# Kernel optimization log

Hardware: AMD Instinct MI355X
Metric: run time of the kernel (lower is better)

The kernel has to match this reference:

```python
import jax, jax.numpy as jnp
import numpy as np

B, L, D = 2, 2048, 1024
H = 16
DH = D // H
FACTOR = 0.6
U = max(1, min(L, int(FACTOR * L)))  # 1228 selected queries


def setup_inputs() -> dict:
    key = jax.random.key(0)
    ks = jax.random.split(key, 9)
    s = 0.02
    return {
        "x": jax.random.normal(ks[0], (B, L, D), dtype=jnp.float32),
        "Wq": jax.random.normal(ks[1], (D, D), dtype=jnp.float32) * s,
        "bq": jnp.zeros((D,), dtype=jnp.float32),
        "Wk": jax.random.normal(ks[2], (D, D), dtype=jnp.float32) * s,
        "bk": jnp.zeros((D,), dtype=jnp.float32),
        "Wv": jax.random.normal(ks[3], (D, D), dtype=jnp.float32) * s,
        "bv": jnp.zeros((D,), dtype=jnp.float32),
        "Wo": jax.random.normal(ks[4], (D, D), dtype=jnp.float32) * s,
        "bo": jnp.zeros((D,), dtype=jnp.float32),
    }


def _split_heads(x):
    b, l, d = x.shape
    return x.reshape(b, l, H, DH).transpose(0, 2, 1, 3)  # [b,h,l,dh]


def reference(x, Wq, bq, Wk, bk, Wv, bv, Wo, bo):
    b, l, _ = x.shape
    scale = 1.0 / jnp.sqrt(jnp.asarray(DH, dtype=x.dtype))

    q = _split_heads(x @ Wq + bq)  # [b,h,l,dh]
    k = _split_heads(x @ Wk + bk)
    v = _split_heads(x @ Wv + bv)

    # full scores for sparsity heuristic
    scores = jnp.einsum("bhqd,bhkd->bhqk", q, k) * scale  # [b,h,l,l]
    sparsity = scores.max(axis=-1) - scores.mean(axis=-1)  # [b,h,l]

    _, top_idx = jax.lax.top_k(sparsity, U)  # [b,h,U]

    # gather selected queries, attend only on those rows
    q_sel = jnp.take_along_axis(q, top_idx[..., None], axis=2)  # [b,h,U,dh]
    scores_sel = jnp.einsum("bhud,bhkd->bhuk", q_sel, k) * scale  # [b,h,U,l]
    attn = jax.nn.softmax(scores_sel, axis=-1)
    out_sel = jnp.einsum("bhuk,bhkd->bhud", attn, v)  # [b,h,U,dh]

    # scatter back into zero-initialized output
    bi = jnp.arange(b)[:, None, None]
    hi = jnp.arange(H)[None, :, None]
    out = jnp.zeros_like(q).at[bi, hi, top_idx].set(out_sel)  # [b,h,l,dh]

    out = out.transpose(0, 2, 1, 3).reshape(b, l, D)
    return out @ Wo + bo
```

## Files before the change

kernel.cpp:

```cpp
#include <hip/hip_runtime.h>
#include <math.h>
#include <stdint.h>

#define Bn 2
#define Ln 2048
#define Dn 1024
#define Hn 16
#define DHn 64
#define Un 1228
#define BHn (Bn*Hn)
#define SCALE 0.125f
#define SXf 16.0f
#define SWf 256.0f
#define SQf 16.0f
#define SVf 16.0f
#define SPf 16.0f
#define ESC_PROJ (1.0f / 4096.0f)
#define ESC_OUT  (1.0f / 65536.0f)
#define PSC (SCALE / 256.0f)

typedef _Float16 f16;
typedef __attribute__((ext_vector_type(8))) _Float16 f16x8;
typedef __attribute__((ext_vector_type(4))) float f32x4;
struct h4s { f16 x, y, z, w; };

__device__ __forceinline__ void splitf16(float f, f16& hi, f16& lo) {
  hi = (f16)f;
  lo = (f16)(f - (float)hi);
}

__device__ __forceinline__ void gl_lds16(const void* g, void* l) {
  __builtin_amdgcn_global_load_lds(
      (const __attribute__((address_space(1))) void*)g,
      (__attribute__((address_space(3))) void*)l, 16, 0, 0);
}

#define MFMA(a, b, c) __builtin_amdgcn_mfma_f32_16x16x32_f16((a), (b), (c), 0, 0, 0)

__global__ __launch_bounds__(256) void split_kernel(
    const float* __restrict__ in, f16* __restrict__ oh, f16* __restrict__ ol, int n4) {
  int i = blockIdx.x * 256 + threadIdx.x;
  if (i >= n4) return;
  float4 v = ((const float4*)in)[i];
  h4s h, l;
  splitf16(v.x * SXf, h.x, l.x); splitf16(v.y * SXf, h.y, l.y);
  splitf16(v.z * SXf, h.z, l.z); splitf16(v.w * SXf, h.w, l.w);
  ((h4s*)oh)[i] = h; ((h4s*)ol)[i] = l;
}

__global__ __launch_bounds__(256) void tsplit_w4(
    const float* __restrict__ W0, const float* __restrict__ W1,
    const float* __restrict__ W2, const float* __restrict__ W3,
    f16* __restrict__ oh, f16* __restrict__ ol) {
  __shared__ float ts[64][65];
  const int t = threadIdx.x;
  const int r0 = blockIdx.x * 64, c0 = blockIdx.y * 64;
  const int z = blockIdx.z;
  const float* in = (z == 0) ? W0 : (z == 1) ? W1 : (z == 2) ? W2 : W3;
#pragma unroll
  for (int c = 0; c < 4; ++c) {
    int f = (c * 256 + t) * 4; int row = f >> 6, col = f & 63;
    float4 v = *(const float4*)&in[(size_t)(r0 + row) * Dn + c0 + col];
    ts[row][col] = v.x; ts[row][col + 1] = v.y; ts[row][col + 2] = v.z; ts[row][col + 3] = v.w;
  }
  __syncthreads();
#pragma unroll
  for (int c = 0; c < 4; ++c) {
    int f = (c * 256 + t) * 4; int crow = f >> 6, rcol = f & 63;
    h4s h, l;
    splitf16(ts[rcol + 0][crow] * SWf, h.x, l.x);
    splitf16(ts[rcol + 1][crow] * SWf, h.y, l.y);
    splitf16(ts[rcol + 2][crow] * SWf, h.z, l.z);
    splitf16(ts[rcol + 3][crow] * SWf, h.w, l.w);
    size_t o = (size_t)(z * 1024 + c0 + crow) * Dn + r0 + rcol;
    *(h4s*)&oh[o] = h; *(h4s*)&ol[o] = l;
  }
}

__global__ void gemm_qkv(
    const f16* __restrict__ Ah, const f16* __restrict__ Al,
    const f16* __restrict__ Bth, const f16* __restrict__ Btl,
    const float* __restrict__ bq, const float* __restrict__ bk, const float* __restrict__ bv,
    float* __restrict__ Qf, f16* __restrict__ Qbh, f16* __restrict__ Qbl,
    float* __restrict__ Kf, f16* __restrict__ Kbh, f16* __restrict__ Kbl,
    f16* __restrict__ Vh16, int K) {
  __shared__ f16 sAh[128 * 32], sAl[128 * 32], sBh[128 * 32], sBl[128 * 32];
  const int t = threadIdx.x;
  const int w = t >> 6, lane = t & 63, lm = lane & 15, q = lane >> 4;
  const int wr = w >> 1, wc = w & 1;
  const int n0 = blockIdx.x * 128, m0 = blockIdx.y * 128;
  f32x4 acc[4][4] = {};
  for (int k0 = 0; k0 < K; k0 += 32) {
    const f16* s0 = Ah + (size_t)m0 * K + k0;
    const f16* s1 = Al + (size_t)m0 * K + k0;
    const f16* s2 = Bth + (size_t)n0 * K + k0;
    const f16* s3 = Btl + (size_t)n0 * K + k0;
#pragma unroll
    for (int c = 0; c < 2; ++c) {
      int f = (c * 256 + t) * 8; int row = f >> 5, col = f & 31;
      size_t go = (size_t)row * K + col;
      gl_lds16(s0 + go, &sAh[f]);
      gl_lds16(s1 + go, &sAl[f]);
      gl_lds16(s2 + go, &sBh[f]);
      gl_lds16(s3 + go, &sBl[f]);
    }
    __syncthreads();
    f16x8 a_h[4], a_l[4], b_h[4], b_l[4];
#pragma unroll
    for (int mi = 0; mi < 4; ++mi) {
      int r = (wr * 64 + mi * 16 + lm) * 32 + q * 8;
      a_h[mi] = *(const f16x8*)&sAh[r];
      a_l[mi] = *(const f16x8*)&sAl[r];
    }
#pragma unroll
    for (int ni = 0; ni < 4; ++ni) {
      int r = (wc * 64 + ni * 16 + lm) * 32 + q * 8;
      b_h[ni] = *(const f16x8*)&sBh[r];
      b_l[ni] = *(const f16x8*)&sBl[r];
    }
#pragma unroll
    for (int mi = 0; mi < 4; ++mi)
#pragma unroll
      for (int ni = 0; ni < 4; ++ni) {
        acc[mi][ni] = MFMA(a_h[mi], b_h[ni], acc[mi][ni]);
        acc[mi][ni] = MFMA(a_h[mi], b_l[ni], acc[mi][ni]);
        acc[mi][ni] = MFMA(a_l[mi], b_h[ni], acc[mi][ni]);
      }
    __syncthreads();
  }
#pragma unroll
  for (int mi = 0; mi < 4; ++mi)
#pragma unroll
    for (int ni = 0; ni < 4; ++ni) {
      int nglob = n0 + wc * 64 + ni * 16;
      int seg = nglob >> 10;
      int c = (nglob & 1023) + lm;
      const float* bp = (seg == 0) ? bq : (seg == 1) ? bk : bv;
      float bvv = bp[c];
#pragma unroll
      for (int r = 0; r < 4; ++r) {
        int grow = m0 + wr * 64 + mi * 16 + q * 4 + r;
        float v = acc[mi][ni][r] * ESC_PROJ + bvv;
        size_t o = (size_t)grow * 1024 + c;
        if (seg == 0) {
          Qf[o] = v;
          f16 hh, ll; splitf16(v * SQf, hh, ll); Qbh[o] = hh; Qbl[o] = ll;
        } else if (seg == 1) {
          Kf[o] = v;
          f16 hh, ll; splitf16(v * SQf, hh, ll); Kbh[o] = hh; Kbl[o] = ll;
        } else {
          Vh16[o] = (f16)(v * SVf);
        }
      }
    }
}

__global__ __launch_bounds__(256) void tsplit_v(
    const f16* __restrict__ Vh16, f16* __restrict__ out) {
  __shared__ f16 ts[64][72];
  const int t = threadIdx.x;
  const int l0 = blockIdx.x * 64;
  const int bh = blockIdx.y, b = bh >> 4, h = bh & 15;
#pragma unroll
  for (int c = 0; c < 2; ++c) {
    int e = c * 256 + t; int row = e >> 3, cg = e & 7;
    *(uint4*)&ts[row][cg * 8] =
        *(const uint4*)&Vh16[((size_t)b * Ln + l0 + row) * Dn + h * DHn + cg * 8];
  }
  __syncthreads();
#pragma unroll
  for (int c = 0; c < 2; ++c) {
    int e = c * 256 + t; int drow = e >> 3, lg = e & 7;
    f16 tmp[8];
#pragma unroll
    for (int j = 0; j < 8; ++j) tmp[j] = ts[lg * 8 + j][drow];
    *(uint4*)&out[((size_t)bh * DHn + drow) * Ln + l0 + lg * 8] = *(uint4*)tmp;
  }
}

__global__ __launch_bounds__(256, 4) void gemm_a1(
    const f16* __restrict__ A,
    const f16* __restrict__ Bth, const f16* __restrict__ Btl,
    const float* __restrict__ bias, float escale,
    float* __restrict__ Cf, int M, int N, int K) {
  __shared__ f16 sA[128 * 32], sBh[64 * 32], sBl[64 * 32];
  const int t = threadIdx.x;
  const int w = t >> 6, lane = t & 63, lm = lane & 15, q = lane >> 4;
  const int wr = w >> 1, wc = w & 1;
  const int n0 = blockIdx.x * 64, m0 = blockIdx.y * 128;
  f32x4 acc[4][2] = {};
  for (int k0 = 0; k0 < K; k0 += 32) {
    const f16* s0 = A + (size_t)m0 * K + k0;
    const f16* s2 = Bth + (size_t)n0 * K + k0;
    const f16* s3 = Btl + (size_t)n0 * K + k0;
#pragma unroll
    for (int c = 0; c < 2; ++c) {
      int f = (c * 256 + t) * 8; int row = f >> 5, col = f & 31;
      gl_lds16(s0 + (size_t)row * K + col, &sA[f]);
    }
    {
      int f = t * 8; int row = f >> 5, col = f & 31;
      gl_lds16(s2 + (size_t)row * K + col, &sBh[f]);
      gl_lds16(s3 + (size_t)row * K + col, &sBl[f]);
    }
    __syncthreads();
    f16x8 a_[4], b_h[2], b_l[2];
#pragma unroll
    for (int mi = 0; mi < 4; ++mi)
      a_[mi] = *(const f16x8*)&sA[(wr * 64 + mi * 16 + lm) * 32 + q * 8];
#pragma unroll
    for (int ni = 0; ni < 2; ++ni) {
      int r = (wc * 32 + ni * 16 + lm) * 32 + q * 8;
      b_h[ni] = *(const f16x8*)&sBh[r];
      b_l[ni] = *(const f16x8*)&sBl[r];
    }
#pragma unroll
    for (int mi = 0; mi < 4; ++mi)
#pragma unroll
      for (int ni = 0; ni < 2; ++ni) {
        acc[mi][ni] = MFMA(a_[mi], b_h[ni], acc[mi][ni]);
        acc[mi][ni] = MFMA(a_[mi], b_l[ni], acc[mi][ni]);
      }
    __syncthreads();
  }
#pragma unroll
  for (int mi = 0; mi < 4; ++mi)
#pragma unroll
    for (int ni = 0; ni < 2; ++ni) {
      int gcol = n0 + wc * 32 + ni * 16 + lm;
      float bvv = bias[gcol];
#pragma unroll
      for (int r = 0; r < 4; ++r) {
        int grow = m0 + wr * 64 + mi * 16 + q * 4 + r;
        Cf[(size_t)grow * N + gcol] = acc[mi][ni][r] * escale + bvv;
      }
    }
}

__global__ __launch_bounds__(256) void ksum_part(
    const f16* __restrict__ Kh, const f16* __restrict__ Kl, float* __restrict__ ksum) {
  __shared__ float red[4][64];
  const int t = threadIdx.x, d = t & 63, seg = t >> 6;
  const int bx = blockIdx.x, bh = blockIdx.y, b = bh >> 4, h = bh & 15;
  float s = 0.f;
  const int lbase = bx * 256 + seg * 64;
  for (int r = 0; r < 64; ++r) {
    size_t o = ((size_t)b * Ln + lbase + r) * Dn + h * DHn + d;
    s += (float)Kh[o] + (float)Kl[o];
  }
  red[seg][d] = s;
  __syncthreads();
  if (t < 64) atomicAdd(&ksum[bh * DHn + t], red[0][t] + red[1][t] + red[2][t] + red[3][t]);
}

__global__ __launch_bounds__(256, 2) void attn_stats_mfma(
    const f16* __restrict__ Qh, const f16* __restrict__ Ql,
    const f16* __restrict__ Kh, const f16* __restrict__ Kl,
    const float* __restrict__ ksum,
    float* __restrict__ row_max, float* __restrict__ spars) {
  __shared__ f16 sQh[128 * 64], sQl[128 * 64], sKh[128 * 64], sKl[128 * 64];
  __shared__ float redm[128][5];
  const int t = threadIdx.x;
  const int w = t >> 6, lane = t & 63, lm = lane & 15, q = lane >> 4;
  const int bh = blockIdx.y, b = bh >> 4, h = bh & 15;
  const int q0 = blockIdx.x * 128;
  const f16* qsh = Qh + ((size_t)b * Ln + q0) * Dn + h * DHn;
  const f16* qsl = Ql + ((size_t)b * Ln + q0) * Dn + h * DHn;
#pragma unroll
  for (int c = 0; c < 4; ++c) {
    int f = (c * 256 + t) * 8; int row = f >> 6, col = f & 63;
    size_t go = (size_t)row * Dn + col;
    gl_lds16(qsh + go, &sQh[f]);
    gl_lds16(qsl + go, &sQl[f]);
  }
  __syncthreads();
  f16x8 a_h[8][2], a_l[8][2];
#pragma unroll
  for (int mi = 0; mi < 8; ++mi)
#pragma unroll
    for (int ks = 0; ks < 2; ++ks) {
      int r = (mi * 16 + lm) * 64 + ks * 32 + q * 8;
      a_h[mi][ks] = *(const f16x8*)&sQh[r];
      a_l[mi][ks] = *(const f16x8*)&sQl[r];
    }
  float rmax[8][4];
#pragma unroll
  for (int mi = 0; mi < 8; ++mi)
#pragma unroll
    for (int r = 0; r < 4; ++r) rmax[mi][r] = -1e30f;

  for (int kt = 0; kt < Ln / 128; ++kt) {
    __syncthreads();
    const f16* ksh = Kh + ((size_t)b * Ln + kt * 128) * Dn + h * DHn;
    const f16* ksl = Kl + ((size_t)b * Ln + kt * 128) * Dn + h * DHn;
#pragma unroll
    for (int c = 0; c < 4; ++c) {
      int f = (c * 256 + t) * 8; int row = f >> 6, col = f & 63;
      size_t go = (size_t)row * Dn + col;
      gl_lds16(ksh + go, &sKh[f]);
      gl_lds16(ksl + go, &sKl[f]);
    }
    __syncthreads();
#pragma unroll
    for (int ni = 0; ni < 2; ++ni) {
      int bcol = (w * 2 + ni) * 16;
      f16x8 b_h[2], b_l[2];
#pragma unroll
      for (int ks = 0; ks < 2; ++ks) {
        int r = (bcol + lm) * 64 + ks * 32 + q * 8;
        b_h[ks] = *(const f16x8*)&sKh[r];
        b_l[ks] = *(const f16x8*)&sKl[r];
      }
#pragma unroll
      for (int mi = 0; mi < 8; ++mi) {
        f32x4 acc = {0.f, 0.f, 0.f, 0.f};
#pragma unroll
        for (int ks = 0; ks < 2; ++ks) {
          acc = MFMA(a_h[mi][ks], b_h[ks], acc);
          acc = MFMA(a_h[mi][ks], b_l[ks], acc);
          acc = MFMA(a_l[mi][ks], b_h[ks], acc);
        }
#pragma unroll
        for (int r = 0; r < 4; ++r) rmax[mi][r] = fmaxf(rmax[mi][r], acc[r]);
      }
    }
  }
#pragma unroll
  for (int mi = 0; mi < 8; ++mi)
#pragma unroll
    for (int r = 0; r < 4; ++r) {
      float v = rmax[mi][r];
      v = fmaxf(v, __shfl_xor(v, 1)); v = fmaxf(v, __shfl_xor(v, 2));
      v = fmaxf(v, __shfl_xor(v, 4)); v = fmaxf(v, __shfl_xor(v, 8));
      if (lm == 0) redm[mi * 16 + q * 4 + r][w] = v;
    }
  __syncthreads();
  if (t < 128) {
    float m = fmaxf(fmaxf(redm[t][0], redm[t][1]), fmaxf(redm[t][2], redm[t][3]));
    float dot = 0.f;
    const float* kp = ksum + bh * DHn;
#pragma unroll
    for (int d = 0; d < 64; ++d)
      dot += ((float)sQh[t * 64 + d] + (float)sQl[t * 64 + d]) * kp[d];
    row_max[(size_t)bh * Ln + q0 + t] = m * PSC;
    spars[(size_t)bh * Ln + q0 + t] = m * PSC - dot * (PSC / (float)Ln);
  }
}

__global__ __launch_bounds__(1024) void topk_sort(
    const float* __restrict__ spars, int* __restrict__ top_idx, int* __restrict__ wrow) {
  __shared__ unsigned long long keys[Ln];
  const int t = threadIdx.x;
  const int bh = blockIdx.x;
  for (int i = t; i < Ln; i += 1024) {
    unsigned u = __float_as_uint(spars[(size_t)bh * Ln + i]);
    u = (u & 0x80000000u) ? ~u : (u | 0x80000000u);
    u = ~u;
    keys[i] = ((unsigned long long)u << 32) | (unsigned)i;
  }
  __syncthreads();
  for (int k = 2; k <= Ln; k <<= 1) {
    for (int j = k >> 1; j > 0; j >>= 1) {
      int i = ((t & ~(j - 1)) << 1) | (t & (j - 1));
      int ixj = i | j;
      unsigned long long a = keys[i], bb = keys[ixj];
      bool up = ((i & k) == 0);
      if ((a > bb) == up) { keys[i] = bb; keys[ixj] = a; }
      __syncthreads();
    }
  }
  for (int u = t; u < Un - 8; u += 1024)
    top_idx[(size_t)bh * Un + u] = (int)(keys[u] & 0xFFFFFFFFu);
  if (t < 16) wrow[bh * 16 + t] = (int)(keys[Un - 8 + t] & 0xFFFFFFFFu);
}

__global__ __launch_bounds__(256) void refine_rows(
    const float* __restrict__ Qf, const float* __restrict__ Kf,
    const int* __restrict__ wrow, float* __restrict__ spx) {
  __shared__ float qs[64];
  __shared__ float redm[4], reds[4];
  const int t = threadIdx.x;
  const int j = blockIdx.x, bh = blockIdx.y, b = bh >> 4, h = bh & 15;
  const int qi = wrow[bh * 16 + j];
  if (t < 64) qs[t] = Qf[((size_t)b * Ln + qi) * Dn + h * DHn + t];
  __syncthreads();
  float mx = -1e30f, sm = 0.f;
  for (int ki = t; ki < Ln; ki += 256) {
    const float* kp = &Kf[((size_t)b * Ln + ki) * Dn + h * DHn];
    float s = 0.f;
#pragma unroll
    for (int d0 = 0; d0 < 64; d0 += 4) {
      float4 k4 = *(const float4*)&kp[d0];
      s = fmaf(k4.x, qs[d0], s);
      s = fmaf(k4.y, qs[d0 + 1], s);
      s = fmaf(k4.z, qs[d0 + 2], s);
      s = fmaf(k4.w, qs[d0 + 3], s);
    }
    mx = fmaxf(mx, s); sm += s;
  }
  const int w = t >> 6, lane = t & 63;
#pragma unroll
  for (int off = 1; off < 64; off <<= 1) {
    mx = fmaxf(mx, __shfl_xor(mx, off));
    sm += __shfl_xor(sm, off);
  }
  if (lane == 0) { redm[w] = mx; reds[w] = sm; }
  __syncthreads();
  if (t == 0) {
    float m = fmaxf(fmaxf(redm[0], redm[1]), fmaxf(redm[2], redm[3]));
    float s = reds[0] + reds[1] + reds[2] + reds[3];
    spx[bh * 16 + j] = SCALE * (m - s * (1.0f / (float)Ln));
  }
}

__global__ __launch_bounds__(64) void topk_final(
    const float* __restrict__ spx, const int* __restrict__ wrow,
    int* __restrict__ top_idx) {
  const int bh = blockIdx.x;
  if (threadIdx.x != 0) return;
  float v[16]; int r[16];
#pragma unroll
  for (int j = 0; j < 16; ++j) { v[j] = spx[bh * 16 + j]; r[j] = wrow[bh * 16 + j]; }
  unsigned taken = 0;
  for (int s = 0; s < 8; ++s) {
    int best = -1;
    for (int j = 0; j < 16; ++j) {
      if (taken & (1u << j)) continue;
      if (best < 0 || v[j] > v[best] || (v[j] == v[best] && r[j] < r[best])) best = j;
    }
    taken |= 1u << best;
    top_idx[(size_t)bh * Un + (Un - 8) + s] = r[best];
  }
}

__global__ __launch_bounds__(256, 4) void attn_sel_part(
    const f16* __restrict__ Qh, const f16* __restrict__ Kh,
    const f16* __restrict__ Vth,
    const int* __restrict__ topi, const float* __restrict__ row_max,
    float* __restrict__ pO, float* __restrict__ pD) {
  __shared__ f16 sK[64 * 64], sV[64 * 64];
  __shared__ f16 sQP[64 * 80];
  __shared__ float rmL[64];
  __shared__ int qxL[64];
  __shared__ float dred[64][5];
  const int t = threadIdx.x;
  const int w = t >> 6, lane = t & 63, lm = lane & 15, q = lane >> 4;
  const int half = blockIdx.y & 1, bh = blockIdx.y >> 1, b = bh >> 4, h = bh & 15;
  const int u0 = blockIdx.x * 64;
  const int nrows = (Un - u0 < 64) ? (Un - u0) : 64;
  if (t < 64) {
    int qi = topi[(size_t)bh * Un + ((t < nrows) ? (u0 + t) : 0)];
    qxL[t] = qi;
    rmL[t] = row_max[(size_t)bh * Ln + qi];
  }
  __syncthreads();
#pragma unroll
  for (int c = 0; c < 2; ++c) {
    int f = (c * 256 + t) * 8; int row = f >> 6, col = f & 63;
    size_t go = ((size_t)b * Ln + qxL[row]) * Dn + h * DHn + col;
    *(uint4*)&sQP[row * 80 + col] = *(const uint4*)&Qh[go];
  }
  __syncthreads();
  f16x8 aq[4][2];
#pragma unroll
  for (int mi = 0; mi < 4; ++mi)
#pragma unroll
    for (int ks = 0; ks < 2; ++ks)
      aq[mi][ks] = *(const f16x8*)&sQP[(mi * 16 + lm) * 80 + ks * 32 + q * 8];
  f32x4 oacc[4] = {};
  float dacc[4][4] = {};

  const f16* kbase = Kh + (size_t)b * Ln * Dn + h * DHn;
  const f16* vbase = Vth + (size_t)bh * DHn * Ln;
  for (int kt = 0; kt < 16; ++kt) {
    const int l0 = half * 1024 + kt * 64;
    __syncthreads();
#pragma unroll
    for (int c = 0; c < 2; ++c) {
      int f = (c * 256 + t) * 8; int row = f >> 6, col = f & 63;
      gl_lds16(kbase + (size_t)(l0 + row) * Dn + col, &sK[f]);
      gl_lds16(vbase + (size_t)row * Ln + l0 + col, &sV[f]);
    }
    __syncthreads();
    f16x8 kb[2];
#pragma unroll
    for (int ks = 0; ks < 2; ++ks)
      kb[ks] = *(const f16x8*)&sK[(w * 16 + lm) * 64 + ks * 32 + q * 8];
#pragma unroll
    for (int mi = 0; mi < 4; ++mi) {
      f32x4 acc = {0.f, 0.f, 0.f, 0.f};
      acc = MFMA(aq[mi][0], kb[0], acc);
      acc = MFMA(aq[mi][1], kb[1], acc);
#pragma unroll
      for (int r = 0; r < 4; ++r) {
        int row = mi * 16 + q * 4 + r;
        float p = __expf(acc[r] * PSC - rmL[row]);
        dacc[mi][r] += p;
        sQP[row * 80 + w * 16 + lm] = (f16)(p * SPf);
      }
    }
    __syncthreads();
    f16x8 vb[2];
#pragma unroll
    for (int ks = 0; ks < 2; ++ks)
      vb[ks] = *(const f16x8*)&sV[(w * 16 + lm) * 64 + ks * 32 + q * 8];
#pragma unroll
    for (int mi = 0; mi < 4; ++mi) {
#pragma unroll
      for (int ks = 0; ks < 2; ++ks) {
        f16x8 pf = *(const f16x8*)&sQP[(mi * 16 + lm) * 80 + ks * 32 + q * 8];
        oacc[mi] = MFMA(pf, vb[ks], oacc[mi]);
      }
    }
  }
#pragma unroll
  for (int mi = 0; mi < 4; ++mi)
#pragma unroll
    for (int r = 0; r < 4; ++r) {
      float v = dacc[mi][r];
      v += __shfl_xor(v, 1); v += __shfl_xor(v, 2);
      v += __shfl_xor(v, 4); v += __shfl_xor(v, 8);
      if (lm == 0) dred[mi * 16 + q * 4 + r][w] = v;
    }
  __syncthreads();
  const size_t pbase = ((size_t)half * BHn + bh) * 1280 + u0;
  if (t < 64)
    pD[pbase + t] = dred[t][0] + dred[t][1] + dred[t][2] + dred[t][3];
#pragma unroll
  for (int mi = 0; mi < 4; ++mi)
#pragma unroll
    for (int r = 0; r < 4; ++r) {
      int row = mi * 16 + q * 4 + r;
      pO[(pbase + row) * 64 + w * 16 + lm] = oacc[mi][r];
    }
}

__global__ __launch_bounds__(256) void attn_combine(
    const float* __restrict__ pO, const float* __restrict__ pD,
    const int* __restrict__ topi, f16* __restrict__ AOh) {
  const int t = threadIdx.x;
  const int u0 = blockIdx.x * 64, bh = blockIdx.y, b = bh >> 4, h = bh & 15;
  const int nrows = (Un - u0 < 64) ? (Un - u0) : 64;
  const int row = t >> 2, pg = t & 3;
  if (row >= nrows) return;
  int qi = topi[(size_t)bh * Un + u0 + row];
  size_t i0 = (size_t)bh * 1280 + u0 + row;
  size_t i1 = (size_t)BHn * 1280 + i0;
  float dinv = 1.0f / (pD[i0] + pD[i1]);
  const float* p0 = &pO[i0 * 64 + pg * 16];
  const float* p1 = &pO[i1 * 64 + pg * 16];
  f16 buf[16];
#pragma unroll
  for (int c = 0; c < 4; ++c) {
    float4 a = *(const float4*)&p0[c * 4];
    float4 bb = *(const float4*)&p1[c * 4];
    buf[c * 4 + 0] = (f16)((a.x + bb.x) * dinv);
    buf[c * 4 + 1] = (f16)((a.y + bb.y) * dinv);
    buf[c * 4 + 2] = (f16)((a.z + bb.z) * dinv);
    buf[c * 4 + 3] = (f16)((a.w + bb.w) * dinv);
  }
  f16* dst = &AOh[((size_t)b * Ln + qi) * Dn + h * DHn + pg * 16];
  *(uint4*)&dst[0] = *(uint4*)&buf[0];
  *(uint4*)&dst[8] = *(uint4*)&buf[8];
}

extern "C" void kernel_launch(void* const* d_in, const int* in_sizes, int n_in,
                              void* d_out, int out_size, void* d_ws, size_t ws_size,
                              hipStream_t stream) {
  (void)in_sizes; (void)n_in; (void)out_size; (void)ws_size;
  const float* x  = (const float*)d_in[0];
  const float* Wq = (const float*)d_in[1];
  const float* bq = (const float*)d_in[2];
  const float* Wk = (const float*)d_in[3];
  const float* bk = (const float*)d_in[4];
  const float* Wv = (const float*)d_in[5];
  const float* bv = (const float*)d_in[6];
  const float* Wo = (const float*)d_in[7];
  const float* bo = (const float*)d_in[8];
  float* out = (float*)d_out;

  uint8_t* p = (uint8_t*)d_ws;
  const size_t NE = (size_t)Bn * Ln * Dn;
  f16* xh = (f16*)p;  p += NE * 2;
  f16* xl = (f16*)p;  p += NE * 2;
  f16* Wt_h = (f16*)p; p += (size_t)4096 * Dn * 2;
  f16* Wt_l = (f16*)p; p += (size_t)4096 * Dn * 2;
  f16* Qbh = (f16*)p; p += NE * 2;
  f16* Qbl = (f16*)p; p += NE * 2;
  f16* Kbh = (f16*)p; p += NE * 2;
  f16* Kbl = (f16*)p; p += NE * 2;
  float* Qf = (float*)p;  p += NE * 4;
  float* Kf = (float*)p;  p += NE * 4;
  f16* Vh16 = (f16*)p; p += NE * 2;
  f16* Vth  = (f16*)p; p += NE * 2;
  float* rowmax = (float*)p; p += (size_t)BHn * Ln * 4;
  float* spars  = (float*)p; p += (size_t)BHn * Ln * 4;
  float* ksum   = (float*)p; p += (size_t)BHn * DHn * 4;
  int* topi     = (int*)p;   p += (size_t)BHn * Un * 4;
  int* wrow     = (int*)p;   p += (size_t)BHn * 16 * 4;
  float* spx    = (float*)p; p += (size_t)BHn * 16 * 4;
  float* pD     = (float*)p; p += (size_t)2 * BHn * 1280 * 4;
  float* pO = Qf;
  f16* AOh = xh;

  dim3 blk(256);
  hipLaunchKernelGGL(split_kernel, dim3((int)(NE / 4 / 256)), blk, 0, stream, x, xh, xl, (int)(NE / 4));
  hipLaunchKernelGGL(tsplit_w4, dim3(16, 16, 4), blk, 0, stream, Wq, Wk, Wv, Wo, Wt_h, Wt_l);
  hipLaunchKernelGGL(gemm_qkv, dim3(24, 32), blk, 0, stream, xh, xl, Wt_h, Wt_l,
                     bq, bk, bv, Qf, Qbh, Qbl, Kf, Kbh, Kbl, Vh16, Dn);
  hipLaunchKernelGGL(tsplit_v, dim3(Ln / 64, BHn), blk, 0, stream, Vh16, Vth);
  hipMemsetAsync(ksum, 0, (size_t)BHn * DHn * 4, stream);
  hipLaunchKernelGGL(ksum_part, dim3(8, BHn), blk, 0, stream, Kbh, Kbl, ksum);
  hipLaunchKernelGGL(attn_stats_mfma, dim3(Ln / 128, BHn), blk, 0, stream,
                     Qbh, Qbl, Kbh, Kbl, ksum, rowmax, spars);
  hipLaunchKernelGGL(topk_sort, dim3(BHn), dim3(1024), 0, stream, spars, topi, wrow);
  hipLaunchKernelGGL(refine_rows, dim3(16, BHn), blk, 0, stream, Qf, Kf, wrow, spx);
  hipLaunchKernelGGL(topk_final, dim3(BHn), dim3(64), 0, stream, spx, wrow, topi);
  hipMemsetAsync(AOh, 0, NE * 2, stream);
  hipLaunchKernelGGL(attn_sel_part, dim3((Un + 63) / 64, 2 * BHn), blk, 0, stream,
                     Qbh, Kbh, Vth, topi, rowmax, pO, pD);
  hipLaunchKernelGGL(attn_combine, dim3((Un + 63) / 64, BHn), blk, 0, stream,
                     pO, pD, topi, AOh);
  hipLaunchKernelGGL(gemm_a1, dim3(16, 32), blk, 0, stream, AOh,
                     Wt_h + (size_t)3072 * Dn, Wt_l + (size_t)3072 * Dn, bo,
                     ESC_OUT, out, Bn * Ln, Dn, Dn);
}
```

Measured before the change: 406.7 us.

## Drop split-fp16 low parts for Q/K scoring and widen refinement window

Sparsity scoring in attn_stats_mfma now uses plain fp16 Q and K with a single MFMA per k-step instead of three split-precision MFMAs. This removes the Qbl/Kbl buffers and their writes and halves LDS use, which allows higher occupancy (launch bounds raised to 4 blocks). ksum now reads fp32 K directly. To offset the loss of precision near the top-k boundary, the fp32 refinement window grows from 16 to 32 candidate rows. The risk is misselected queries if fp16 error exceeds what the wider window covers.

```diff
diff --git a/kernel.cpp b/kernel.cpp
--- a/kernel.cpp
+++ b/kernel.cpp
@@ -9,6 +9,7 @@
 #define DHn 64
 #define Un 1228
 #define BHn (Bn*Hn)
+#define WIN 32
 #define SCALE 0.125f
 #define SXf 16.0f
 #define SWf 256.0f
@@ -81,8 +82,8 @@
     const f16* __restrict__ Ah, const f16* __restrict__ Al,
     const f16* __restrict__ Bth, const f16* __restrict__ Btl,
     const float* __restrict__ bq, const float* __restrict__ bk, const float* __restrict__ bv,
-    float* __restrict__ Qf, f16* __restrict__ Qbh, f16* __restrict__ Qbl,
-    float* __restrict__ Kf, f16* __restrict__ Kbh, f16* __restrict__ Kbl,
+    float* __restrict__ Qf, f16* __restrict__ Qbh,
+    float* __restrict__ Kf, f16* __restrict__ Kbh,
     f16* __restrict__ Vh16, int K) {
   __shared__ f16 sAh[128 * 32], sAl[128 * 32], sBh[128 * 32], sBl[128 * 32];
   const int t = threadIdx.x;
@@ -144,10 +145,10 @@
         size_t o = (size_t)grow * 1024 + c;
         if (seg == 0) {
           Qf[o] = v;
-          f16 hh, ll; splitf16(v * SQf, hh, ll); Qbh[o] = hh; Qbl[o] = ll;
+          Qbh[o] = (f16)(v * SQf);
         } else if (seg == 1) {
           Kf[o] = v;
-          f16 hh, ll; splitf16(v * SQf, hh, ll); Kbh[o] = hh; Kbl[o] = ll;
+          Kbh[o] = (f16)(v * SQf);
         } else {
           Vh16[o] = (f16)(v * SVf);
         }
@@ -238,51 +239,42 @@
 }
 
 __global__ __launch_bounds__(256) void ksum_part(
-    const f16* __restrict__ Kh, const f16* __restrict__ Kl, float* __restrict__ ksum) {
+    const float* __restrict__ Kf, float* __restrict__ ksum) {
   __shared__ float red[4][64];
   const int t = threadIdx.x, d = t & 63, seg = t >> 6;
   const int bx = blockIdx.x, bh = blockIdx.y, b = bh >> 4, h = bh & 15;
   float s = 0.f;
   const int lbase = bx * 256 + seg * 64;
-  for (int r = 0; r < 64; ++r) {
-    size_t o = ((size_t)b * Ln + lbase + r) * Dn + h * DHn + d;
-    s += (float)Kh[o] + (float)Kl[o];
-  }
+  for (int r = 0; r < 64; ++r)
+    s += Kf[((size_t)b * Ln + lbase + r) * Dn + h * DHn + d];
   red[seg][d] = s;
   __syncthreads();
   if (t < 64) atomicAdd(&ksum[bh * DHn + t], red[0][t] + red[1][t] + red[2][t] + red[3][t]);
 }
 
-__global__ __launch_bounds__(256, 2) void attn_stats_mfma(
-    const f16* __restrict__ Qh, const f16* __restrict__ Ql,
-    const f16* __restrict__ Kh, const f16* __restrict__ Kl,
+__global__ __launch_bounds__(256, 4) void attn_stats_mfma(
+    const f16* __restrict__ Qh, const f16* __restrict__ Kh,
     const float* __restrict__ ksum,
     float* __restrict__ row_max, float* __restrict__ spars) {
-  __shared__ f16 sQh[128 * 64], sQl[128 * 64], sKh[128 * 64], sKl[128 * 64];
+  __shared__ f16 sQ[128 * 64], sK[128 * 64];
   __shared__ float redm[128][5];
   const int t = threadIdx.x;
   const int w = t >> 6, lane = t & 63, lm = lane & 15, q = lane >> 4;
   const int bh = blockIdx.y, b = bh >> 4, h = bh & 15;
   const int q0 = blockIdx.x * 128;
-  const f16* qsh = Qh + ((size_t)b * Ln + q0) * Dn + h * DHn;
-  const f16* qsl = Ql + ((size_t)b * Ln + q0) * Dn + h * DHn;
+  const f16* qs = Qh + ((size_t)b * Ln + q0) * Dn + h * DHn;
 #pragma unroll
   for (int c = 0; c < 4; ++c) {
     int f = (c * 256 + t) * 8; int row = f >> 6, col = f & 63;
-    size_t go = (size_t)row * Dn + col;
-    gl_lds16(qsh + go, &sQh[f]);
-    gl_lds16(qsl + go, &sQl[f]);
-  }
-  __syncthreads();
-  f16x8 a_h[8][2], a_l[8][2];
+    gl_lds16(qs + (size_t)row * Dn + col, &sQ[f]);
+  }
+  __syncthreads();
+  f16x8 a_[8][2];
 #pragma unroll
   for (int mi = 0; mi < 8; ++mi)
 #pragma unroll
-    for (int ks = 0; ks < 2; ++ks) {
-      int r = (mi * 16 + lm) * 64 + ks * 32 + q * 8;
-      a_h[mi][ks] = *(const f16x8*)&sQh[r];
-      a_l[mi][ks] = *(const f16x8*)&sQl[r];
-    }
+    for (int ks = 0; ks < 2; ++ks)
+      a_[mi][ks] = *(const f16x8*)&sQ[(mi * 16 + lm) * 64 + ks * 32 + q * 8];
   float rmax[8][4];
 #pragma unroll
   for (int mi = 0; mi < 8; ++mi)
@@ -291,35 +283,25 @@
 
   for (int kt = 0; kt < Ln / 128; ++kt) {
     __syncthreads();
-    const f16* ksh = Kh + ((size_t)b * Ln + kt * 128) * Dn + h * DHn;
-    const f16* ksl = Kl + ((size_t)b * Ln + kt * 128) * Dn + h * DHn;
+    const f16* ks_ = Kh + ((size_t)b * Ln + kt * 128) * Dn + h * DHn;
 #pragma unroll
     for (int c = 0; c < 4; ++c) {
       int f = (c * 256 + t) * 8; int row = f >> 6, col = f & 63;
-      size_t go = (size_t)row * Dn + col;
-      gl_lds16(ksh + go, &sKh[f]);
-      gl_lds16(ksl + go, &sKl[f]);
+      gl_lds16(ks_ + (size_t)row * Dn + col, &sK[f]);
     }
     __syncthreads();
 #pragma unroll
     for (int ni = 0; ni < 2; ++ni) {
       int bcol = (w * 2 + ni) * 16;
-      f16x8 b_h[2], b_l[2];
-#pragma unroll
-      for (int ks = 0; ks < 2; ++ks) {
-        int r = (bcol + lm) * 64 + ks * 32 + q * 8;
-        b_h[ks] = *(const f16x8*)&sKh[r];
-        b_l[ks] = *(const f16x8*)&sKl[r];
-      }
+      f16x8 b_[2];
+#pragma unroll
+      for (int ks = 0; ks < 2; ++ks)
+        b_[ks] = *(const f16x8*)&sK[(bcol + lm) * 64 + ks * 32 + q * 8];
 #pragma unroll
       for (int mi = 0; mi < 8; ++mi) {
         f32x4 acc = {0.f, 0.f, 0.f, 0.f};
-#pragma unroll
-        for (int ks = 0; ks < 2; ++ks) {
-          acc = MFMA(a_h[mi][ks], b_h[ks], acc);
-          acc = MFMA(a_h[mi][ks], b_l[ks], acc);
-          acc = MFMA(a_l[mi][ks], b_h[ks], acc);
-        }
+        acc = MFMA(a_[mi][0], b_[0], acc);
+        acc = MFMA(a_[mi][1], b_[1], acc);
 #pragma unroll
         for (int r = 0; r < 4; ++r) rmax[mi][r] = fmaxf(rmax[mi][r], acc[r]);
       }
@@ -341,9 +323,9 @@
     const float* kp = ksum + bh * DHn;
 #pragma unroll
     for (int d = 0; d < 64; ++d)
-      dot += ((float)sQh[t * 64 + d] + (float)sQl[t * 64 + d]) * kp[d];
+      dot += (float)sQ[t * 64 + d] * kp[d];
     row_max[(size_t)bh * Ln + q0 + t] = m * PSC;
-    spars[(size_t)bh * Ln + q0 + t] = m * PSC - dot * (PSC / (float)Ln);
+    spars[(size_t)bh * Ln + q0 + t] = m * PSC - dot * (SCALE / (16.0f * (float)Ln));
   }
 }
 
@@ -369,9 +351,9 @@
       __syncthreads();
     }
   }
-  for (int u = t; u < Un - 8; u += 1024)
+  for (int u = t; u < Un - WIN / 2; u += 1024)
     top_idx[(size_t)bh * Un + u] = (int)(keys[u] & 0xFFFFFFFFu);
-  if (t < 16) wrow[bh * 16 + t] = (int)(keys[Un - 8 + t] & 0xFFFFFFFFu);
+  if (t < WIN) wrow[bh * WIN + t] = (int)(keys[Un - WIN / 2 + t] & 0xFFFFFFFFu);
 }
 
 __global__ __launch_bounds__(256) void refine_rows(
@@ -381,7 +363,7 @@
   __shared__ float redm[4], reds[4];
   const int t = threadIdx.x;
   const int j = blockIdx.x, bh = blockIdx.y, b = bh >> 4, h = bh & 15;
-  const int qi = wrow[bh * 16 + j];
+  const int qi = wrow[bh * WIN + j];
   if (t < 64) qs[t] = Qf[((size_t)b * Ln + qi) * Dn + h * DHn + t];
   __syncthreads();
   float mx = -1e30f, sm = 0.f;
@@ -409,7 +391,7 @@
   if (t == 0) {
     float m = fmaxf(fmaxf(redm[0], redm[1]), fmaxf(redm[2], redm[3]));
     float s = reds[0] + reds[1] + reds[2] + reds[3];
-    spx[bh * 16 + j] = SCALE * (m - s * (1.0f / (float)Ln));
+    spx[bh * WIN + j] = SCALE * (m - s * (1.0f / (float)Ln));
   }
 }
 
@@ -418,18 +400,18 @@
     int* __restrict__ top_idx) {
   const int bh = blockIdx.x;
   if (threadIdx.x != 0) return;
-  float v[16]; int r[16];
-#pragma unroll
-  for (int j = 0; j < 16; ++j) { v[j] = spx[bh * 16 + j]; r[j] = wrow[bh * 16 + j]; }
+  float v[WIN]; int r[WIN];
+#pragma unroll
+  for (int j = 0; j < WIN; ++j) { v[j] = spx[bh * WIN + j]; r[j] = wrow[bh * WIN + j]; }
   unsigned taken = 0;
-  for (int s = 0; s < 8; ++s) {
+  for (int s = 0; s < WIN / 2; ++s) {
     int best = -1;
-    for (int j = 0; j < 16; ++j) {
+    for (int j = 0; j < WIN; ++j) {
       if (taken & (1u << j)) continue;
       if (best < 0 || v[j] > v[best] || (v[j] == v[best] && r[j] < r[best])) best = j;
     }
     taken |= 1u << best;
-    top_idx[(size_t)bh * Un + (Un - 8) + s] = r[best];
+    top_idx[(size_t)bh * Un + (Un - WIN / 2) + s] = r[best];
   }
 }
 
@@ -586,9 +568,7 @@
   f16* Wt_h = (f16*)p; p += (size_t)4096 * Dn * 2;
   f16* Wt_l = (f16*)p; p += (size_t)4096 * Dn * 2;
   f16* Qbh = (f16*)p; p += NE * 2;
-  f16* Qbl = (f16*)p; p += NE * 2;
   f16* Kbh = (f16*)p; p += NE * 2;
-  f16* Kbl = (f16*)p; p += NE * 2;
   float* Qf = (float*)p;  p += NE * 4;
   float* Kf = (float*)p;  p += NE * 4;
   f16* Vh16 = (f16*)p; p += NE * 2;
@@ -597,8 +577,8 @@
   float* spars  = (float*)p; p += (size_t)BHn * Ln * 4;
   float* ksum   = (float*)p; p += (size_t)BHn * DHn * 4;
   int* topi     = (int*)p;   p += (size_t)BHn * Un * 4;
-  int* wrow     = (int*)p;   p += (size_t)BHn * 16 * 4;
-  float* spx    = (float*)p; p += (size_t)BHn * 16 * 4;
+  int* wrow     = (int*)p;   p += (size_t)BHn * WIN * 4;
+  float* spx    = (float*)p; p += (size_t)BHn * WIN * 4;
   float* pD     = (float*)p; p += (size_t)2 * BHn * 1280 * 4;
   float* pO = Qf;
   f16* AOh = xh;
@@ -607,14 +587,14 @@
   hipLaunchKernelGGL(split_kernel, dim3((int)(NE / 4 / 256)), blk, 0, stream, x, xh, xl, (int)(NE / 4));
   hipLaunchKernelGGL(tsplit_w4, dim3(16, 16, 4), blk, 0, stream, Wq, Wk, Wv, Wo, Wt_h, Wt_l);
   hipLaunchKernelGGL(gemm_qkv, dim3(24, 32), blk, 0, stream, xh, xl, Wt_h, Wt_l,
-                     bq, bk, bv, Qf, Qbh, Qbl, Kf, Kbh, Kbl, Vh16, Dn);
+                     bq, bk, bv, Qf, Qbh, Kf, Kbh, Vh16, Dn);
   hipLaunchKernelGGL(tsplit_v, dim3(Ln / 64, BHn), blk, 0, stream, Vh16, Vth);
   hipMemsetAsync(ksum, 0, (size_t)BHn * DHn * 4, stream);
-  hipLaunchKernelGGL(ksum_part, dim3(8, BHn), blk, 0, stream, Kbh, Kbl, ksum);
+  hipLaunchKernelGGL(ksum_part, dim3(8, BHn), blk, 0, stream, Kf, ksum);
   hipLaunchKernelGGL(attn_stats_mfma, dim3(Ln / 128, BHn), blk, 0, stream,
-                     Qbh, Qbl, Kbh, Kbl, ksum, rowmax, spars);
+                     Qbh, Kbh, ksum, rowmax, spars);
   hipLaunchKernelGGL(topk_sort, dim3(BHn), dim3(1024), 0, stream, spars, topi, wrow);
-  hipLaunchKernelGGL(refine_rows, dim3(16, BHn), blk, 0, stream, Qf, Kf, wrow, spx);
+  hipLaunchKernelGGL(refine_rows, dim3(WIN, BHn), blk, 0, stream, Qf, Kf, wrow, spx);
   hipLaunchKernelGGL(topk_final, dim3(BHn), dim3(64), 0, stream, spx, wrow, topi);
   hipMemsetAsync(AOh, 0, NE * 2, stream);
   hipLaunchKernelGGL(attn_sel_part, dim3((Un + 63) / 64, 2 * BHn), blk, 0, stream,
```

Result: slower. 525.5 us (+29.2%).
